# Kernel tuning notes

Measured on AMD Instinct MI355X. Metric: run time of the kernel, lower is better.

## Reference

```python
import jax, jax.numpy as jnp
import numpy as np

BATCH, L = 2, 1024
D_MODEL, D_INNER, D_STATE, DT_RANK, K = 2048, 4096, 16, 128, 4


def setup_inputs() -> dict:
    key = jax.random.key(0)
    ks = jax.random.split(key, 9)
    g = lambda i, shape, s: jax.random.normal(ks[i], shape, jnp.float32) * s
    A_log = jnp.log(jnp.broadcast_to(jnp.arange(1, D_STATE + 1, dtype=jnp.float32),
                                     (D_INNER, D_STATE)))
    return {
        "hidden_states": g(0, (BATCH, L, D_MODEL), 1.0),
        "W_in": g(1, (2 * D_INNER, D_MODEL), 0.02),
        "conv_w": g(2, (D_INNER, K), 0.2),
        "conv_b": g(3, (D_INNER,), 0.02),
        "W_x": g(4, (DT_RANK + 2 * D_STATE, D_INNER), 0.02),
        "W_dt": g(5, (D_INNER, DT_RANK), 0.02),
        "b_dt": g(6, (D_INNER,), 0.02),
        "A_log": A_log,
        "D": jnp.ones((D_INNER,), jnp.float32),
        "W_out": g(7, (D_MODEL, D_INNER), 0.02),
        "b_out": g(8, (D_MODEL,), 0.02),
    }


def reference(hidden_states, W_in, conv_w, conv_b, W_x, W_dt, b_dt, A_log, D, W_out, b_out):
    b, l, _ = hidden_states.shape
    # in_proj -> (b, 2*d_inner, l), split into x and gate z
    xz = jnp.einsum('bld,ed->bel', hidden_states, W_in)
    x, z = jnp.split(xz, 2, axis=1)                      # each (b, d_inner, l)
    # conv_state = F.pad(x, (d_conv - l, 0)): keeps the last d_conv timesteps
    conv_state = x[:, :, -K:]
    # causal depthwise conv1d (left pad K-1) + SiLU
    xc = jax.lax.conv_general_dilated(
        x, conv_w[:, None, :], window_strides=(1,), padding=[(K - 1, 0)],
        feature_group_count=D_INNER, dimension_numbers=('NCH', 'OIH', 'NCH'))
    xc = jax.nn.silu(xc + conv_b[None, :, None])         # (b, d_inner, l)
    # x_proj -> dt / B / C
    x_dbl = jnp.einsum('bdl,ed->ble', xc, W_x)           # (b, l, dt_rank+2n)
    dt, Bm, Cm = jnp.split(x_dbl, [DT_RANK, DT_RANK + D_STATE], axis=-1)
    dt = jnp.einsum('blr,dr->bdl', dt, W_dt)             # (b, d_inner, l), no bias here
    delta = jax.nn.softplus(dt + b_dt[None, :, None])    # dt_proj bias folded into softplus
    A = -jnp.exp(A_log)                                  # (d_inner, d_state)

    def step(state, inp):                                # state: (b, d_inner, d_state)
        d_t, b_t, c_t, u_t = inp                         # (b,d), (b,n), (b,n), (b,d)
        dA = jnp.exp(d_t[..., None] * A)                 # (b, d, n)
        state = dA * state + (d_t * u_t)[..., None] * b_t[:, None, :]
        y_t = jnp.einsum('bdn,bn->bd', state, c_t)
        return state, y_t

    xs = (delta.transpose(2, 0, 1),                      # (l, b, d)
          Bm.transpose(1, 0, 2),                         # (l, b, n)
          Cm.transpose(1, 0, 2),
          xc.transpose(2, 0, 1))
    init = jnp.zeros((b, D_INNER, D_STATE), delta.dtype)
    last_state, ys = jax.lax.scan(step, init, xs)
    y = ys.transpose(1, 2, 0) + D[None, :, None] * xc    # (b, d_inner, l) skip term
    y = y * jax.nn.silu(z)                               # gating
    out = jnp.einsum('bdl,ed->ble', y, W_out) + b_out    # (b, l, d_model)
    return out, conv_state, last_state
```

## Files before the change

### kernel.cpp

```cpp
#include <hip/hip_runtime.h>
#include <stdint.h>
#include <stddef.h>

typedef __bf16 bf16;
typedef __attribute__((ext_vector_type(8))) __bf16 bf16x8;
typedef __attribute__((ext_vector_type(4))) float floatx4;

#define GAS __attribute__((address_space(1)))
#define LAS __attribute__((address_space(3)))

__device__ __forceinline__ void async16(const void* g, void* l) {
  __builtin_amdgcn_global_load_lds((const GAS void*)g, (LAS void*)l, 16, 0, 0);
}

__device__ __forceinline__ bf16x8 cvt8(const float* p) {
  floatx4 a = *(const floatx4*)p;
  floatx4 b = *(const floatx4*)(p + 4);
  bf16x8 r;
  r[0] = (bf16)a[0]; r[1] = (bf16)a[1]; r[2] = (bf16)a[2]; r[3] = (bf16)a[3];
  r[4] = (bf16)b[0]; r[5] = (bf16)b[1]; r[6] = (bf16)b[2]; r[7] = (bf16)b[3];
  return r;
}

template <int EPI, int AF, int BF, int TM>
__global__ __launch_bounds__(256, 4) void gemm_bt(
    const void* __restrict__ Aptr, const void* __restrict__ Bptr,
    void* __restrict__ Cout, const float* __restrict__ bias,
    int M, int N, int K, int lda, int ldb) {
  __shared__ bf16 As[TM * 32];
  __shared__ bf16 Bs[128 * 32];
  const int tid = threadIdx.x;

  const int rowBase = blockIdx.x * TM;
  const int colBase = blockIdx.y * 128;
  const int kLen = K / gridDim.z;
  const int k0 = blockIdx.z * kLen;
  const int kIters = kLen / 32;

  const int sRow = tid >> 2;
  const int sCol = (tid & 3) << 3;
  const int wave = tid >> 6;
  const int lane = tid & 63;
  constexpr int MI = 4;
  constexpr int NJ = (TM == 128) ? 4 : 2;
  const int wm = (TM == 128) ? ((wave >> 1) << 6) : 0;
  const int wn = (TM == 128) ? ((wave & 1) << 6) : (wave << 5);
  const int lr = lane & 15;
  const int kg = lane >> 4;

  floatx4 acc[MI][NJ] = {};

  for (int kt = 0; kt < kIters; ++kt) {
    const int kk = k0 + kt * 32;
    __syncthreads();
    if constexpr (AF) {
      const float* pa =
          (const float*)Aptr + (size_t)(rowBase + sRow) * lda + kk + sCol;
      *(bf16x8*)&As[tid * 8] = cvt8(pa);
      if constexpr (TM == 128)
        *(bf16x8*)&As[2048 + tid * 8] = cvt8(pa + (size_t)64 * lda);
    } else {
      const bf16* pa =
          (const bf16*)Aptr + (size_t)(rowBase + sRow) * lda + kk + sCol;
      async16(pa, &As[tid * 8]);
      if constexpr (TM == 128)
        async16(pa + (size_t)64 * lda, &As[2048 + tid * 8]);
    }
    if constexpr (BF) {
      const float* pb =
          (const float*)Bptr + (size_t)(colBase + sRow) * ldb + kk + sCol;
      *(bf16x8*)&Bs[tid * 8] = cvt8(pb);
      *(bf16x8*)&Bs[2048 + tid * 8] = cvt8(pb + (size_t)64 * ldb);
    } else {
      const bf16* pb =
          (const bf16*)Bptr + (size_t)(colBase + sRow) * ldb + kk + sCol;
      async16(pb, &Bs[tid * 8]);
      async16(pb + (size_t)64 * ldb, &Bs[2048 + tid * 8]);
    }
    __syncthreads();

    bf16x8 af[MI], bg[NJ];
#pragma unroll
    for (int i = 0; i < MI; ++i)
      af[i] = *(const bf16x8*)&As[(wm + i * 16 + lr) * 32 + kg * 8];
#pragma unroll
    for (int j = 0; j < NJ; ++j)
      bg[j] = *(const bf16x8*)&Bs[(wn + j * 16 + lr) * 32 + kg * 8];
#pragma unroll
    for (int i = 0; i < MI; ++i)
#pragma unroll
      for (int j = 0; j < NJ; ++j)
        acc[i][j] = __builtin_amdgcn_mfma_f32_16x16x32_bf16(af[i], bg[j],
                                                            acc[i][j], 0, 0, 0);
  }

#pragma unroll
  for (int i = 0; i < MI; ++i) {
#pragma unroll
    for (int j = 0; j < NJ; ++j) {
      const int col = colBase + wn + j * 16 + lr;
      float bv = 0.f;
      if constexpr (EPI == 2 || EPI == 3) bv = bias[col];
#pragma unroll
      for (int r = 0; r < 4; ++r) {
        const int row = rowBase + wm + i * 16 + kg * 4 + r;
        const size_t idx = (size_t)row * N + col;
        float v = acc[i][j][r];
        if constexpr (EPI == 0) {
          ((bf16*)Cout)[idx] = (bf16)v;
        } else if constexpr (EPI == 1) {
          atomicAdd((float*)Cout + idx, v);
        } else if constexpr (EPI == 2) {
          v += bv;
          const float t = __expf(v);
          const float sp = (v > 20.f) ? v : __logf(1.f + t);
          ((bf16*)Cout)[idx] = (bf16)sp;
        } else if constexpr (EPI == 3) {
          ((float*)Cout)[idx] = v + bv;
        } else {
          ((float*)Cout)[(size_t)blockIdx.z * 524288 + idx] = v;
        }
      }
    }
  }
}

__global__ __launch_bounds__(256) void reduce_xdbl(
    const float* __restrict__ part, float* __restrict__ xdbl) {
  const size_t i4 = ((size_t)blockIdx.x * 256 + threadIdx.x) * 4;
  floatx4 s = {};
#pragma unroll
  for (int z = 0; z < 8; ++z) {
    const floatx4 v = *(const floatx4*)&part[(size_t)z * 524288 + i4];
    s[0] += v[0]; s[1] += v[1]; s[2] += v[2]; s[3] += v[3];
  }
  *(floatx4*)&xdbl[i4] = s;
}

#define PC0 524288UL
#define PC1 2621440UL
#define PC2 2686976UL
#define PC3 3735552UL
#define PC4 3866624UL
__global__ __launch_bounds__(256) void prep_all(
    const float* __restrict__ h, const float* __restrict__ wi,
    const float* __restrict__ wd, const float* __restrict__ wo,
    const float* __restrict__ wx, bf16* __restrict__ hb,
    bf16* __restrict__ wib, bf16* __restrict__ wdb, bf16* __restrict__ wob,
    bf16* __restrict__ wxp) {
  const size_t c = (size_t)blockIdx.x * 256 + threadIdx.x;
  if (c < PC0) {
    const size_t e = c * 8;
    *(bf16x8*)&hb[e] = cvt8(&h[e]);
  } else if (c < PC1) {
    const size_t e = (c - PC0) * 8;
    *(bf16x8*)&wib[e] = cvt8(&wi[e]);
  } else if (c < PC2) {
    const size_t e = (c - PC1) * 8;
    *(bf16x8*)&wdb[e] = cvt8(&wd[e]);
  } else if (c < PC3) {
    const size_t e = (c - PC2) * 8;
    *(bf16x8*)&wob[e] = cvt8(&wo[e]);
  } else if (c < PC4) {
    const size_t e = (c - PC3) * 8;
    if ((e >> 12) < 160) {
      *(bf16x8*)&wxp[e] = cvt8(&wx[e]);
    } else {
      bf16x8 z = {};
      *(bf16x8*)&wxp[e] = z;
    }
  }
}

__global__ void wxpad_prep(const float* __restrict__ Wx,
                           bf16* __restrict__ WXPAD) {
  const int idx = blockIdx.x * 256 + threadIdx.x;
  const int row = idx >> 12;
  WXPAD[idx] = (row < 160) ? (bf16)Wx[idx] : (bf16)0.f;
}

__global__ void conv_kernel(const bf16* __restrict__ XZ,
                            const float* __restrict__ conv_w,
                            const float* __restrict__ conv_b,
                            bf16* __restrict__ XC,
                            float* __restrict__ outConv) {
  const int idx = blockIdx.x * 256 + threadIdx.x;
  const int d = idx & 4095;
  const int row = idx >> 12;
  const int l = row & 1023;
  float acc = conv_b[d];
#pragma unroll
  for (int k = 0; k < 4; ++k) {
    if (l - 3 + k >= 0)
      acc += conv_w[d * 4 + k] * (float)XZ[(size_t)(row - 3 + k) * 8192 + d];
  }
  const float s = acc / (1.f + __expf(-acc));
  XC[(size_t)row * 4096 + d] = (bf16)s;
  if (idx < 32768) {
    const int k = idx & 3;
    const int dd = (idx >> 2) & 4095;
    const int b = idx >> 14;
    outConv[idx] = (float)XZ[(size_t)(b * 1024 + 1020 + k) * 8192 + dd];
  }
}

#define NCH 32
#define CLEN 32
#define LOG2E 1.44269504088896f

__global__ __launch_bounds__(256) void scan_phase1(
    const bf16* __restrict__ DELTA, const bf16* __restrict__ XC,
    const float* __restrict__ XDBL, const float* __restrict__ A_log,
    bf16* __restrict__ P, bf16* __restrict__ Lc) {
  const int bd = blockIdx.x * 256 + threadIdx.x;
  const int c = blockIdx.y;
  const int b = bd >> 12;
  const int d = bd & 4095;
  float A2[16], st[16], p[16];
#pragma unroll
  for (int n = 0; n < 16; ++n) {
    A2[n] = -__expf(A_log[d * 16 + n]) * LOG2E;
    st[n] = 0.f;
    p[n] = 1.f;
  }
  size_t row = (size_t)b * 1024 + (size_t)c * CLEN;
  for (int t = 0; t < CLEN; ++t, ++row) {
    const float dlt = (float)DELTA[row * 4096 + d];
    const float u = (float)XC[row * 4096 + d];
    const float* __restrict__ Bp = XDBL + row * 256 + 128;
    const float du = dlt * u;
#pragma unroll
    for (int n = 0; n < 16; ++n) {
      const float dA = exp2f(dlt * A2[n]);
      st[n] = dA * st[n] + du * Bp[n];
      p[n] *= dA;
    }
  }
  const size_t o = ((size_t)c * 8192 + bd) * 16;
  bf16x8 pk[2], lk[2];
#pragma unroll
  for (int n = 0; n < 16; ++n) {
    pk[n >> 3][n & 7] = (bf16)p[n];
    lk[n >> 3][n & 7] = (bf16)st[n];
  }
  *(bf16x8*)&P[o] = pk[0];
  *(bf16x8*)&P[o + 8] = pk[1];
  *(bf16x8*)&Lc[o] = lk[0];
  *(bf16x8*)&Lc[o + 8] = lk[1];
}

__global__ __launch_bounds__(256) void scan_phase2(
    const bf16* __restrict__ P, const bf16* __restrict__ Lc,
    float* __restrict__ In, float* __restrict__ lastOut) {
  const int bd = blockIdx.x * 256 + threadIdx.x;
  float st[16] = {};
  for (int c = 0; c < NCH; ++c) {
    const size_t o = ((size_t)c * 8192 + bd) * 16;
    const bf16x8 p0 = *(const bf16x8*)&P[o];
    const bf16x8 p1 = *(const bf16x8*)&P[o + 8];
    const bf16x8 l0 = *(const bf16x8*)&Lc[o];
    const bf16x8 l1 = *(const bf16x8*)&Lc[o + 8];
    floatx4 w[4];
#pragma unroll
    for (int n = 0; n < 16; ++n) w[n >> 2][n & 3] = st[n];
#pragma unroll
    for (int q = 0; q < 4; ++q) *(floatx4*)&In[o + q * 4] = w[q];
#pragma unroll
    for (int n = 0; n < 8; ++n) {
      st[n] = (float)p0[n] * st[n] + (float)l0[n];
      st[8 + n] = (float)p1[n] * st[8 + n] + (float)l1[n];
    }
  }
  const int b = bd >> 12;
  const int d = bd & 4095;
#pragma unroll
  for (int n = 0; n < 16; ++n)
    lastOut[(size_t)b * 65536 + d * 16 + n] = st[n];
}

__global__ __launch_bounds__(256) void scan_phase3(
    const bf16* __restrict__ DELTA, const bf16* __restrict__ XC,
    const bf16* __restrict__ XZ, const float* __restrict__ XDBL,
    const float* __restrict__ A_log, const float* __restrict__ Dp,
    const float* __restrict__ In, bf16* __restrict__ Y) {
  const int bd = blockIdx.x * 256 + threadIdx.x;
  const int c = blockIdx.y;
  const int b = bd >> 12;
  const int d = bd & 4095;
  float A2[16], st[16];
  const size_t o = ((size_t)c * 8192 + bd) * 16;
#pragma unroll
  for (int q = 0; q < 4; ++q) {
    const floatx4 v = *(const floatx4*)&In[o + q * 4];
#pragma unroll
    for (int j = 0; j < 4; ++j) st[q * 4 + j] = v[j];
  }
#pragma unroll
  for (int n = 0; n < 16; ++n)
    A2[n] = -__expf(A_log[d * 16 + n]) * LOG2E;
  const float Dd = Dp[d];
  size_t row = (size_t)b * 1024 + (size_t)c * CLEN;
  for (int t = 0; t < CLEN; ++t, ++row) {
    const float dlt = (float)DELTA[row * 4096 + d];
    const float u = (float)XC[row * 4096 + d];
    const float z = (float)XZ[row * 8192 + 4096 + d];
    const float* __restrict__ Bp = XDBL + row * 256 + 128;
    const float du = dlt * u;
    float y = 0.f;
#pragma unroll
    for (int n = 0; n < 16; ++n) {
      const float dA = exp2f(dlt * A2[n]);
      st[n] = dA * st[n] + du * Bp[n];
      y += st[n] * Bp[16 + n];
    }
    const float sig = 1.f / (1.f + __expf(-z));
    Y[row * 4096 + d] = (bf16)((y + Dd * u) * (z * sig));
  }
}

#define OFF_XZ 0UL
#define OFF_XC 33554432UL
#define OFF_DELTA 50331648UL
#define OFF_Y 83886080UL
#define OFF_XDBL 100663296UL
#define OFF_WXPAD 103284736UL
#define OFF_P 105381888UL
#define OFF_L 113770496UL
#define OFF_HBF 122159104UL
#define OFF_WINBF 130547712UL
#define OFF_WDTBF 164102144UL
#define OFF_WOUTBF 165150720UL
#define WS_NEED_CAST 181927936UL

extern "C" void kernel_launch(void* const* d_in, const int* in_sizes, int n_in,
                              void* d_out, int out_size, void* d_ws,
                              size_t ws_size, hipStream_t stream) {
  const float* hidden = (const float*)d_in[0];
  const float* W_in = (const float*)d_in[1];
  const float* conv_w = (const float*)d_in[2];
  const float* conv_b = (const float*)d_in[3];
  const float* W_x = (const float*)d_in[4];
  const float* W_dt = (const float*)d_in[5];
  const float* b_dt = (const float*)d_in[6];
  const float* A_log = (const float*)d_in[7];
  const float* Dvec = (const float*)d_in[8];
  const float* W_out = (const float*)d_in[9];
  const float* b_out = (const float*)d_in[10];

  char* ws = (char*)d_ws;
  bf16* XZ = (bf16*)(ws + OFF_XZ);
  bf16* XC = (bf16*)(ws + OFF_XC);
  bf16* DELTA = (bf16*)(ws + OFF_DELTA);
  float* PART = (float*)(ws + OFF_DELTA + 16777216UL);
  bf16* Y = (bf16*)(ws + OFF_Y);
  float* XDBL = (float*)(ws + OFF_XDBL);
  bf16* WXPAD = (bf16*)(ws + OFF_WXPAD);
  bf16* P = (bf16*)(ws + OFF_P);
  bf16* Lc = (bf16*)(ws + OFF_L);

  float* out = (float*)d_out;
  float* out_conv = out + 4194304;
  float* out_last = out + 4227072;
  float* In = out;

  const bool castOK = ws_size >= WS_NEED_CAST;
  if (castOK) {
    bf16* HBF = (bf16*)(ws + OFF_HBF);
    bf16* WINBF = (bf16*)(ws + OFF_WINBF);
    bf16* WDTBF = (bf16*)(ws + OFF_WDTBF);
    bf16* WOUTBF = (bf16*)(ws + OFF_WOUTBF);
    prep_all<<<15104, 256, 0, stream>>>(hidden, W_in, W_dt, W_out, W_x, HBF,
                                        WINBF, WDTBF, WOUTBF, WXPAD);
    gemm_bt<0, 0, 0, 128><<<dim3(16, 64, 1), 256, 0, stream>>>(
        HBF, WINBF, XZ, nullptr, 2048, 8192, 2048, 2048, 2048);
    conv_kernel<<<32768, 256, 0, stream>>>(XZ, conv_w, conv_b, XC, out_conv);
    gemm_bt<4, 0, 0, 64><<<dim3(32, 2, 8), 256, 0, stream>>>(
        XC, WXPAD, PART, nullptr, 2048, 256, 4096, 4096, 4096);
    reduce_xdbl<<<512, 256, 0, stream>>>(PART, XDBL);
    gemm_bt<2, 1, 0, 64><<<dim3(32, 32, 1), 256, 0, stream>>>(
        XDBL, WDTBF, DELTA, b_dt, 2048, 4096, 128, 256, 128);
    scan_phase1<<<dim3(32, NCH), 256, 0, stream>>>(DELTA, XC, XDBL, A_log, P,
                                                   Lc);
    scan_phase2<<<32, 256, 0, stream>>>(P, Lc, In, out_last);
    scan_phase3<<<dim3(32, NCH), 256, 0, stream>>>(DELTA, XC, XZ, XDBL, A_log,
                                                   Dvec, In, Y);
    gemm_bt<3, 0, 0, 128><<<dim3(16, 16, 1), 256, 0, stream>>>(
        Y, WOUTBF, out, b_out, 2048, 2048, 4096, 4096, 4096);
  } else {
    wxpad_prep<<<4096, 256, 0, stream>>>(W_x, WXPAD);
    gemm_bt<0, 1, 1, 128><<<dim3(16, 64, 1), 256, 0, stream>>>(
        hidden, W_in, XZ, nullptr, 2048, 8192, 2048, 2048, 2048);
    conv_kernel<<<32768, 256, 0, stream>>>(XZ, conv_w, conv_b, XC, out_conv);
    gemm_bt<4, 0, 0, 64><<<dim3(32, 2, 8), 256, 0, stream>>>(
        XC, WXPAD, PART, nullptr, 2048, 256, 4096, 4096, 4096);
    reduce_xdbl<<<512, 256, 0, stream>>>(PART, XDBL);
    gemm_bt<2, 1, 1, 64><<<dim3(32, 32, 1), 256, 0, stream>>>(
        XDBL, W_dt, DELTA, b_dt, 2048, 4096, 128, 256, 128);
    scan_phase1<<<dim3(32, NCH), 256, 0, stream>>>(DELTA, XC, XDBL, A_log, P,
                                                   Lc);
    scan_phase2<<<32, 256, 0, stream>>>(P, Lc, In, out_last);
    scan_phase3<<<dim3(32, NCH), 256, 0, stream>>>(DELTA, XC, XZ, XDBL, A_log,
                                                   Dvec, In, Y);
    gemm_bt<3, 0, 1, 128><<<dim3(16, 16, 1), 256, 0, stream>>>(
        Y, W_out, out, b_out, 2048, 2048, 4096, 4096, 4096);
  }
}
```

Before: 528.1 us.

## Replace in_proj GEMM with 256x256-tile 8-wave ping-pong pipelined kernel

Adds a new bf16 GEMM kernel for the in_proj that uses 256x256 block tiles, 512 threads, double-buffered LDS filled by async global-to-LDS loads with XOR swizzling, and an 8-phase schedule that interleaves staging with MFMA work and uses setprio. It targets the memory-bound, low-reuse 128-tile version by raising arithmetic intensity and overlapping loads with compute. In exchange it uses 128KB of LDS per block, gives only 256 blocks on the GPU, and writes bf16 output with scattered stores. That output store assumes XZ is a bf16 buffer.

```diff
diff --git a/kernel.cpp b/kernel.cpp
--- a/kernel.cpp
+++ b/kernel.cpp
@@ -20,6 +20,118 @@
   r[0] = (bf16)a[0]; r[1] = (bf16)a[1]; r[2] = (bf16)a[2]; r[3] = (bf16)a[3];
   r[4] = (bf16)b[0]; r[5] = (bf16)b[1]; r[6] = (bf16)b[2]; r[7] = (bf16)b[3];
   return r;
+}
+
+__global__ __launch_bounds__(512, 2) void gemm256_8p(
+    const bf16* __restrict__ A, const bf16* __restrict__ B,
+    bf16* __restrict__ C, int M, int N, int K, int lda, int ldb) {
+  __shared__ __attribute__((aligned(16))) bf16 SA[2][2][8192];
+  __shared__ __attribute__((aligned(16))) bf16 SB[2][2][8192];
+
+  const int tid = threadIdx.x;
+  const int wave = tid >> 6;
+  const int lane = tid & 63;
+  const int lr = lane & 15;
+  const int kg = lane >> 4;
+  const int wm = (wave >> 2) * 128;
+  const int wn = (wave & 3) * 64;
+
+  const int tilesM = M >> 8;
+  const int tm = blockIdx.x % tilesM;
+  const int tn = blockIdx.x / tilesM;
+  const int rowBase = tm * 256;
+  const int colBase = tn * 256;
+
+  const int srow = tid >> 2;
+  const int ske = (tid & 3) << 3;
+  const int skel = ske ^ (((srow >> 3) & 1) << 4);
+  const size_t aRow0 = (size_t)(rowBase + srow) * lda;
+  const size_t aRow1 = aRow0 + (size_t)128 * lda;
+  const size_t bRow0 = (size_t)(colBase + srow) * ldb;
+  const size_t bRow1 = bRow0 + (size_t)128 * ldb;
+
+  const int NT = K >> 6;
+
+  const int keSh = (kg << 3) ^ (((lr >> 3) & 1) << 4);
+
+  floatx4 acc[8][4] = {};
+
+  auto stA = [&](int buf, int kh, int kt) {
+    const int gk = kt * 64 + kh * 32 + skel;
+    bf16* d = &SA[buf][kh][0];
+    async16(A + aRow0 + gk, d + tid * 8);
+    async16(A + aRow1 + gk, d + 4096 + tid * 8);
+  };
+  auto stB = [&](int buf, int kh, int kt) {
+    const int gk = kt * 64 + kh * 32 + skel;
+    bf16* d = &SB[buf][kh][0];
+    async16(B + bRow0 + gk, d + tid * 8);
+    async16(B + bRow1 + gk, d + 4096 + tid * 8);
+  };
+
+  stB(0, 0, 0); stA(0, 0, 0); stB(0, 1, 0); stA(0, 1, 0);
+  stB(1, 0, 1); stA(1, 0, 1); stB(1, 1, 1);
+  asm volatile("s_waitcnt vmcnt(6)" ::: "memory");
+  __builtin_amdgcn_s_barrier();
+
+  bf16x8 bg[4], af[4];
+
+#define PH(BUF, KH, MH, DOB, STG, VM)                                          \
+  {                                                                            \
+    const bf16* Ar_ = &SA[BUF][KH][0];                                         \
+    if constexpr (DOB) {                                                       \
+      const bf16* Br_ = &SB[BUF][KH][0];                                       \
+      _Pragma("unroll") for (int n = 0; n < 4; ++n)                            \
+          bg[n] = *(const bf16x8*)&Br_[(wn + n * 16 + lr) * 32 + keSh];        \
+    }                                                                          \
+    _Pragma("unroll") for (int m = 0; m < 4; ++m)                              \
+        af[m] =                                                                \
+            *(const bf16x8*)&Ar_[(wm + ((MH)*4 + m) * 16 + lr) * 32 + keSh];   \
+    STG;                                                                       \
+    __builtin_amdgcn_s_barrier();                                              \
+    asm volatile("s_waitcnt lgkmcnt(0)" ::: "memory");                         \
+    __builtin_amdgcn_sched_barrier(0);                                         \
+    __builtin_amdgcn_s_setprio(1);                                             \
+    _Pragma("unroll") for (int m = 0; m < 4; ++m)                              \
+      _Pragma("unroll") for (int n = 0; n < 4; ++n)                            \
+          acc[(MH)*4 + m][n] = __builtin_amdgcn_mfma_f32_16x16x32_bf16(        \
+              af[m], bg[n], acc[(MH)*4 + m][n], 0, 0, 0);                      \
+    __builtin_amdgcn_s_setprio(0);                                             \
+    if constexpr (VM) asm volatile("s_waitcnt vmcnt(6)" ::: "memory");         \
+    __builtin_amdgcn_s_barrier();                                              \
+  }
+
+  for (int it = 0; it < (NT >> 1); ++it) {
+    const int T0 = it * 2;
+    const int T1 = T0 + 1;
+    const int s1 = (T0 + 2 < NT) ? T0 + 2 : NT - 1;
+    const int s2 = (T1 + 2 < NT) ? T1 + 2 : NT - 1;
+
+    PH(0, 0, 0, true,  stA(1, 1, T1), false)
+    PH(0, 0, 1, false, stB(0, 0, s1), false)
+    PH(0, 1, 0, true,  stA(0, 0, s1), false)
+    PH(0, 1, 1, false, stB(0, 1, s1), true)
+    PH(1, 0, 0, true,  stA(0, 1, s1), false)
+    PH(1, 0, 1, false, stB(1, 0, s2), false)
+    PH(1, 1, 0, true,  stA(1, 0, s2), false)
+    PH(1, 1, 1, false, stB(1, 1, s2), true)
+  }
+#undef PH
+
+  asm volatile("s_waitcnt vmcnt(0)" ::: "memory");
+
+#pragma unroll
+  for (int m = 0; m < 8; ++m) {
+#pragma unroll
+    for (int n = 0; n < 4; ++n) {
+      const int col = colBase + wn + n * 16 + lr;
+#pragma unroll
+      for (int r = 0; r < 4; ++r) {
+        const int row = rowBase + wm + m * 16 + kg * 4 + r;
+        C[(size_t)row * N + col] = (bf16)acc[m][n][r];
+      }
+    }
+  }
 }
 
 template <int EPI, int AF, int BF, int TM>
@@ -371,8 +483,8 @@
     bf16* WOUTBF = (bf16*)(ws + OFF_WOUTBF);
     prep_all<<<15104, 256, 0, stream>>>(hidden, W_in, W_dt, W_out, W_x, HBF,
                                         WINBF, WDTBF, WOUTBF, WXPAD);
-    gemm_bt<0, 0, 0, 128><<<dim3(16, 64, 1), 256, 0, stream>>>(
-        HBF, WINBF, XZ, nullptr, 2048, 8192, 2048, 2048, 2048);
+    gemm256_8p<<<dim3(256), 512, 0, stream>>>(HBF, WINBF, XZ, 2048, 8192,
+                                              2048, 2048, 2048);
     conv_kernel<<<32768, 256, 0, stream>>>(XZ, conv_w, conv_b, XC, out_conv);
     gemm_bt<4, 0, 0, 64><<<dim3(32, 2, 8), 256, 0, stream>>>(
         XC, WXPAD, PART, nullptr, 2048, 256, 4096, 4096, 4096);
```

Result: no change. 519.3 us (-1.7%).
